# Kernel tuning notes

Hardware: AMD Instinct MI355X
Metric: run time of the kernel (lower is better)

Reference implementation:

```python
import jax, jax.numpy as jnp
import numpy as np

N_NODES = 100000
N_EDGES = 3200000
IN_C, HID_C, OUT_C = 128, 16, 5
NEG_SLOPE = 0.2


def setup_inputs() -> dict:
    key = jax.random.key(0)
    ks = jax.random.split(key, 12)
    x = jax.random.normal(ks[0], (N_NODES, IN_C), dtype=jnp.float32)
    edge_index = jax.random.randint(ks[1], (2, N_EDGES), 0, N_NODES, dtype=jnp.int64)
    # GATConv layer 1 params (heads=1)
    s1 = 1.0 / np.sqrt(IN_C)
    W1 = jax.random.uniform(ks[2], (IN_C, HID_C), jnp.float32, -s1, s1)
    att_src1 = jax.random.uniform(ks[3], (HID_C,), jnp.float32, -1.0, 1.0) * s1
    att_dst1 = jax.random.uniform(ks[4], (HID_C,), jnp.float32, -1.0, 1.0) * s1
    b1 = jnp.zeros((HID_C,), jnp.float32)
    # GATConv layer 2 params
    s2 = 1.0 / np.sqrt(HID_C)
    W2 = jax.random.uniform(ks[5], (HID_C, OUT_C), jnp.float32, -s2, s2)
    att_src2 = jax.random.uniform(ks[6], (OUT_C,), jnp.float32, -1.0, 1.0) * s2
    att_dst2 = jax.random.uniform(ks[7], (OUT_C,), jnp.float32, -1.0, 1.0) * s2
    b2 = jnp.zeros((OUT_C,), jnp.float32)
    return {"x": x, "edge_index": edge_index,
            "W1": W1, "att_src1": att_src1, "att_dst1": att_dst1, "b1": b1,
            "W2": W2, "att_src2": att_src2, "att_dst2": att_dst2, "b2": b2}


def gat_layer(x, src, dst, W, att_src, att_dst, bias, n_nodes):
    # project: [N, C_out]
    h = x @ W
    a_src = h @ att_src  # [N]
    a_dst = h @ att_dst  # [N]
    e = a_src[src] + a_dst[dst]            # [E]
    e = jax.nn.leaky_relu(e, NEG_SLOPE)
    # per-destination-node softmax over incoming edges (stable)
    m = jax.ops.segment_max(e, dst, num_segments=n_nodes)
    ex = jnp.exp(e - m[dst])
    denom = jax.ops.segment_sum(ex, dst, num_segments=n_nodes)
    alpha = ex / (denom[dst] + 1e-16)      # [E]
    # weighted scatter-aggregate of source features
    out = jax.ops.segment_sum(h[src] * alpha[:, None], dst, num_segments=n_nodes)
    return out + bias


def reference(x, edge_index, W1, att_src1, att_dst1, b1, W2, att_src2, att_dst2, b2):
    n = x.shape[0]
    loops = jnp.arange(n, dtype=edge_index.dtype)
    src = jnp.concatenate([edge_index[0], loops])  # add_self_loops=True
    dst = jnp.concatenate([edge_index[1], loops])
    h = gat_layer(x, src, dst, W1, att_src1, att_dst1, b1, n)
    h = jax.nn.relu(h)
    h = gat_layer(h, src, dst, W2, att_src2, att_dst2, b2, n)
    return jax.nn.log_softmax(h, axis=1)
```

## Files before the change

### kernel.cpp

```cpp
#include <hip/hip_runtime.h>
#include <hip/hip_fp16.h>

#define N_NODES 100000
#define N_EDGES 3200000
#define E_TOT   (N_EDGES + N_NODES)
#define IN_C 128
#define HID  16
#define OUTC 5
#define NEG_SLOPE 0.2f

#define NBKT 391
#define CAP  9216
#define P1_TILE 8192
#define P1_GRID ((E_TOT + P1_TILE - 1) / P1_TILE)

__device__ __forceinline__ float pk_half2(float a, float b) {
    __half2 h = __halves2half2(__float2half(a), __float2half(b));
    return *(float*)&h;
}
__device__ __forceinline__ float2 unpk_half2(float v) {
    return __half22float2(*(__half2*)&v);
}

__global__ void zero_gcnt_k(int* __restrict__ gcnt) {
    int i = blockIdx.x * blockDim.x + threadIdx.x;
    if (i < NBKT) gcnt[i] = 0;
}

__global__ __launch_bounds__(256) void part_k(const int* __restrict__ ei,
                                              int* __restrict__ gcnt,
                                              unsigned* __restrict__ pairs) {
    __shared__ unsigned vbuf[P1_TILE];
    __shared__ unsigned short bbuf[P1_TILE];
    __shared__ int hist[NBKT];
    __shared__ int cur[NBKT];
    int t = threadIdx.x;
    for (int i = t; i < NBKT; i += 256) hist[i] = 0;
    __syncthreads();
    int base = blockIdx.x * P1_TILE;
    int lim = E_TOT - base; if (lim > P1_TILE) lim = P1_TILE;
    for (int i = t; i < lim; i += 256) {
        int e = base + i;
        int s, d;
        if (e < N_EDGES) { s = ei[e]; d = ei[N_EDGES + e]; }
        else             { s = e - N_EDGES; d = s; }
        int b = d >> 8;
        vbuf[i] = ((unsigned)s << 8) | (unsigned)(d & 255);
        bbuf[i] = (unsigned short)b;
        atomicAdd(&hist[b], 1);
    }
    __syncthreads();
    for (int i = t; i < NBKT; i += 256) {
        int h = hist[i];
        cur[i] = h ? atomicAdd(&gcnt[i], h) : 0;
    }
    __syncthreads();
    for (int i = t; i < lim; i += 256) {
        int b = bbuf[i];
        int p = atomicAdd(&cur[b], 1);
        if (p >= 0 && p < CAP) pairs[(size_t)b * CAP + p] = vbuf[i];
    }
}

__global__ void scan_gcnt_k(const int* __restrict__ gcnt, int* __restrict__ cbase) {
    __shared__ int s[512];
    int t = threadIdx.x;
    int v = (t < NBKT) ? gcnt[t] : 0;
    s[t] = v; __syncthreads();
    for (int off = 1; off < 512; off <<= 1) {
        int x = (t >= off) ? s[t - off] : 0;
        __syncthreads();
        s[t] += x;
        __syncthreads();
    }
    if (t < NBKT) cbase[t] = s[t] - v;
}

__global__ __launch_bounds__(256) void build_k(const unsigned* __restrict__ pairs,
                                               const int* __restrict__ gcnt,
                                               const int* __restrict__ cbase,
                                               int* __restrict__ csr,
                                               int* __restrict__ row_start,
                                               int* __restrict__ cnt) {
    __shared__ int c[256], s[256], cur[256];
    int t = threadIdx.x;
    int b = blockIdx.x;
    c[t] = 0;
    __syncthreads();
    int tot = gcnt[b];
    if (tot > CAP) tot = CAP;
    size_t pbase = (size_t)b * CAP;
    for (int i = t; i < tot; i += 256) atomicAdd(&c[pairs[pbase + i] & 255u], 1);
    __syncthreads();
    int v0 = c[t];
    s[t] = v0; __syncthreads();
    for (int off = 1; off < 256; off <<= 1) {
        int x = (t >= off) ? s[t - off] : 0;
        __syncthreads();
        s[t] += x;
        __syncthreads();
    }
    int excl = s[t] - v0;
    int gbase = cbase[b];
    int node = (b << 8) + t;
    if (node < N_NODES) { row_start[node] = gbase + excl; cnt[node] = v0; }
    cur[t] = gbase + excl;
    __syncthreads();
    for (int i = t; i < tot; i += 256) {
        unsigned v = pairs[pbase + i];
        int pos = atomicAdd(&cur[v & 255u], 1);
        csr[pos] = (int)(v >> 8);
    }
}

__global__ void proj1_k(const float* __restrict__ x, const float* __restrict__ W1,
                        const float* __restrict__ att_s, const float* __restrict__ att_d,
                        __half* __restrict__ h1f, float* __restrict__ a_src,
                        float* __restrict__ a_dst) {
    __shared__ float sW[IN_C * HID];
    __shared__ float sX[16 * IN_C];
    __shared__ float sH[16 * HID];
    int t = threadIdx.x;
    for (int i = t; i < IN_C * HID; i += 256) sW[i] = W1[i];
    int node0 = blockIdx.x * 16;
    for (int i = t; i < 16 * IN_C; i += 256) {
        int r = i >> 7, c = i & 127;
        int node = node0 + r;
        sX[i] = (node < N_NODES) ? x[(size_t)node * IN_C + c] : 0.0f;
    }
    __syncthreads();
    int r = t >> 4, c = t & 15;
    int node = node0 + r;
    float acc = 0.0f;
    #pragma unroll 8
    for (int k = 0; k < IN_C; ++k) acc += sX[r * IN_C + k] * sW[k * HID + c];
    sH[r * HID + c] = acc;
    if (node < N_NODES) h1f[(size_t)node * HID + c] = __float2half(acc);
    __syncthreads();
    if (c == 0 && node < N_NODES) {
        float s = 0.0f, d = 0.0f;
        #pragma unroll
        for (int k = 0; k < HID; ++k) {
            float hv = sH[r * HID + k];
            s += hv * att_s[k];
            d += hv * att_d[k];
        }
        a_src[node] = s;
        a_dst[node] = d;
    }
}

__global__ __launch_bounds__(256) void gat1_k(
    const int* __restrict__ csr, const int* __restrict__ row_start,
    const int* __restrict__ cnt, const __half* __restrict__ h1f,
    const float* __restrict__ a_src1, const float* __restrict__ a_dst1,
    const float* __restrict__ b1, const float* __restrict__ W2,
    const float* __restrict__ as2, const float* __restrict__ ad2,
    float4* __restrict__ h2p, float* __restrict__ a_dst2) {
    __shared__ float sW2[HID * OUTC];
    __shared__ float sB1[HID];
    __shared__ float sAs[OUTC], sAd[OUTC];
    int t = threadIdx.x;
    if (t < HID * OUTC) sW2[t] = W2[t];
    if (t < HID) sB1[t] = b1[t];
    if (t < OUTC) { sAs[t] = as2[t]; sAd[t] = ad2[t]; }
    __syncthreads();

    int node = (blockIdx.x * 256 + t) >> 4;
    int lane = t & 15;
    int start = row_start[node];
    int len   = cnt[node];
    float ad  = a_dst1[node];

    float acc[HID];
    #pragma unroll
    for (int c = 0; c < HID; ++c) acc[c] = 0.0f;
    float accd = 0.0f;
    for (int it = lane; it < len; it += 16) {
        int s = csr[start + it];
        float v = a_src1[s] + ad;
        v = (v > 0.0f) ? v : NEG_SLOPE * v;
        float ex = __expf(v);
        accd += ex;
        const float4* hp = (const float4*)(h1f + (size_t)s * HID);
        float4 r0 = hp[0], r1 = hp[1];
        float2 f0 = unpk_half2(r0.x), f1 = unpk_half2(r0.y);
        float2 f2 = unpk_half2(r0.z), f3 = unpk_half2(r0.w);
        float2 f4 = unpk_half2(r1.x), f5 = unpk_half2(r1.y);
        float2 f6 = unpk_half2(r1.z), f7 = unpk_half2(r1.w);
        acc[0]  += ex * f0.x; acc[1]  += ex * f0.y;
        acc[2]  += ex * f1.x; acc[3]  += ex * f1.y;
        acc[4]  += ex * f2.x; acc[5]  += ex * f2.y;
        acc[6]  += ex * f3.x; acc[7]  += ex * f3.y;
        acc[8]  += ex * f4.x; acc[9]  += ex * f4.y;
        acc[10] += ex * f5.x; acc[11] += ex * f5.y;
        acc[12] += ex * f6.x; acc[13] += ex * f6.y;
        acc[14] += ex * f7.x; acc[15] += ex * f7.y;
    }
    #pragma unroll
    for (int off = 8; off; off >>= 1) {
        accd += __shfl_xor(accd, off);
        #pragma unroll
        for (int c = 0; c < HID; ++c) acc[c] += __shfl_xor(acc[c], off);
    }
    if (lane == 0) {
        float inv = 1.0f / (accd + 1e-16f);
        float g[HID];
        #pragma unroll
        for (int k = 0; k < HID; ++k) g[k] = fmaxf(acc[k] * inv + sB1[k], 0.0f);
        float h2[OUTC];
        #pragma unroll
        for (int c = 0; c < OUTC; ++c) {
            float a = 0.0f;
            #pragma unroll
            for (int k = 0; k < HID; ++k) a += g[k] * sW2[k * OUTC + c];
            h2[c] = a;
        }
        float s2 = 0.0f, d2 = 0.0f;
        #pragma unroll
        for (int c = 0; c < OUTC; ++c) { s2 += h2[c] * sAs[c]; d2 += h2[c] * sAd[c]; }
        a_dst2[node] = d2;
        float4 r;
        r.x = s2;
        r.y = pk_half2(h2[0], h2[1]);
        r.z = pk_half2(h2[2], h2[3]);
        r.w = pk_half2(h2[4], 0.0f);
        h2p[node] = r;
    }
}

__global__ __launch_bounds__(256) void gat2_k(
    const int* __restrict__ csr, const int* __restrict__ row_start,
    const int* __restrict__ cnt, const float4* __restrict__ h2p,
    const float* __restrict__ a_dst2, const float* __restrict__ b2,
    float* __restrict__ out) {
    __shared__ float sB2[OUTC];
    int t = threadIdx.x;
    if (t < OUTC) sB2[t] = b2[t];
    __syncthreads();

    int node = (blockIdx.x * 256 + t) >> 4;
    int lane = t & 15;
    int start = row_start[node];
    int len   = cnt[node];
    float ad  = a_dst2[node];

    float acc[OUTC];
    #pragma unroll
    for (int c = 0; c < OUTC; ++c) acc[c] = 0.0f;
    float accd = 0.0f;
    for (int it = lane; it < len; it += 16) {
        int s = csr[start + it];
        float4 r = h2p[s];
        float v = r.x + ad;
        v = (v > 0.0f) ? v : NEG_SLOPE * v;
        float ex = __expf(v);
        accd += ex;
        float2 f01 = unpk_half2(r.y);
        float2 f23 = unpk_half2(r.z);
        float2 f4_ = unpk_half2(r.w);
        acc[0] += ex * f01.x; acc[1] += ex * f01.y;
        acc[2] += ex * f23.x; acc[3] += ex * f23.y;
        acc[4] += ex * f4_.x;
    }
    #pragma unroll
    for (int off = 8; off; off >>= 1) {
        accd += __shfl_xor(accd, off);
        #pragma unroll
        for (int c = 0; c < OUTC; ++c) acc[c] += __shfl_xor(acc[c], off);
    }
    if (lane == 0) {
        float inv = 1.0f / (accd + 1e-16f);
        float val[OUTC];
        float mx = -3.4e38f;
        #pragma unroll
        for (int c = 0; c < OUTC; ++c) {
            val[c] = acc[c] * inv + sB2[c];
            mx = fmaxf(mx, val[c]);
        }
        float se = 0.0f;
        #pragma unroll
        for (int c = 0; c < OUTC; ++c) se += __expf(val[c] - mx);
        float lse = logf(se) + mx;
        #pragma unroll
        for (int c = 0; c < OUTC; ++c)
            out[(size_t)node * OUTC + c] = val[c] - lse;
    }
}

extern "C" void kernel_launch(void* const* d_in, const int* in_sizes, int n_in,
                              void* d_out, int out_size, void* d_ws, size_t ws_size,
                              hipStream_t stream) {
    const float* x    = (const float*)d_in[0];
    const int*   ei   = (const int*)d_in[1];
    const float* W1   = (const float*)d_in[2];
    const float* as1  = (const float*)d_in[3];
    const float* ad1  = (const float*)d_in[4];
    const float* b1   = (const float*)d_in[5];
    const float* W2   = (const float*)d_in[6];
    const float* as2  = (const float*)d_in[7];
    const float* ad2  = (const float*)d_in[8];
    const float* b2   = (const float*)d_in[9];
    float* out = (float*)d_out;

    char* wsb = (char*)d_ws;
    unsigned* pairs = (unsigned*)wsb;
    __half* h1f     = (__half*)wsb;
    float4* h2p     = (float4*)(wsb + 3200000);
    float*  asrc1   = (float*)(wsb + 4800000);
    float*  adst1   = asrc1 + N_NODES;
    float*  adst2   = adst1 + N_NODES;
    int* csr       = (int*)(wsb + (size_t)NBKT * CAP * 4);
    int* cnt       = csr + E_TOT;
    int* row_start = cnt + N_NODES;
    int* gcnt      = row_start + N_NODES;
    int* cbase     = gcnt + NBKT;

    const int B = 256;
    const int gW = (N_NODES * 16) / B;

    zero_gcnt_k<<<(NBKT + B - 1) / B, B, 0, stream>>>(gcnt);
    part_k<<<P1_GRID, B, 0, stream>>>(ei, gcnt, pairs);
    scan_gcnt_k<<<1, 512, 0, stream>>>(gcnt, cbase);
    build_k<<<NBKT, B, 0, stream>>>(pairs, gcnt, cbase, csr, row_start, cnt);

    proj1_k<<<(N_NODES + 15) / 16, 256, 0, stream>>>(x, W1, as1, ad1, h1f, asrc1, adst1);
    gat1_k<<<gW, B, 0, stream>>>(csr, row_start, cnt, h1f, asrc1, adst1, b1,
                                 W2, as2, ad2, h2p, adst2);
    gat2_k<<<gW, B, 0, stream>>>(csr, row_start, cnt, h2p, adst2, b2, out);
}
```

Before: 274.3 us.

## Drop global CSR build; bucket-local CSR in shared memory inside GAT kernels

Removes the scan and build kernels and the global CSR arrays. Each GAT layer now rebuilds a per-half-bucket CSR in LDS from the partitioned pairs, then aggregates. The edge partition and the layer-1 projection are merged into one launch as disjoint block ranges, and the projection now loads with float4. This trades the global CSR write and read plus two launches for redundant pair scans in both layers, a HCAP limit in LDS, and only 782 blocks per aggregation kernel, which means lower parallelism and more LDS per block.

```diff
diff --git a/kernel.cpp b/kernel.cpp
--- a/kernel.cpp
+++ b/kernel.cpp
@@ -11,8 +11,10 @@
 
 #define NBKT 391
 #define CAP  9216
-#define P1_TILE 8192
-#define P1_GRID ((E_TOT + P1_TILE - 1) / P1_TILE)
+#define HCAP 4736
+#define P_TILE 8192
+#define PART_GRID ((E_TOT + P_TILE - 1) / P_TILE)
+#define PROJ_GRID ((N_NODES + 15) / 16)
 
 __device__ __forceinline__ float pk_half2(float a, float b) {
     __half2 h = __halves2half2(__float2half(a), __float2half(b));
@@ -27,264 +29,298 @@
     if (i < NBKT) gcnt[i] = 0;
 }
 
-__global__ __launch_bounds__(256) void part_k(const int* __restrict__ ei,
-                                              int* __restrict__ gcnt,
-                                              unsigned* __restrict__ pairs) {
-    __shared__ unsigned vbuf[P1_TILE];
-    __shared__ unsigned short bbuf[P1_TILE];
-    __shared__ int hist[NBKT];
-    __shared__ int cur[NBKT];
+__global__ __launch_bounds__(256) void partproj_k(
+    const int* __restrict__ ei, int* __restrict__ gcnt, unsigned* __restrict__ pairs,
+    const float* __restrict__ x, const float* __restrict__ W1,
+    const float* __restrict__ att_s, const float* __restrict__ att_d,
+    __half* __restrict__ h1f, float* __restrict__ a_src, float* __restrict__ a_dst) {
+    __shared__ __align__(16) char smem[52288];
     int t = threadIdx.x;
-    for (int i = t; i < NBKT; i += 256) hist[i] = 0;
-    __syncthreads();
-    int base = blockIdx.x * P1_TILE;
-    int lim = E_TOT - base; if (lim > P1_TILE) lim = P1_TILE;
-    for (int i = t; i < lim; i += 256) {
-        int e = base + i;
-        int s, d;
-        if (e < N_EDGES) { s = ei[e]; d = ei[N_EDGES + e]; }
-        else             { s = e - N_EDGES; d = s; }
-        int b = d >> 8;
-        vbuf[i] = ((unsigned)s << 8) | (unsigned)(d & 255);
-        bbuf[i] = (unsigned short)b;
-        atomicAdd(&hist[b], 1);
-    }
-    __syncthreads();
-    for (int i = t; i < NBKT; i += 256) {
-        int h = hist[i];
-        cur[i] = h ? atomicAdd(&gcnt[i], h) : 0;
-    }
-    __syncthreads();
-    for (int i = t; i < lim; i += 256) {
-        int b = bbuf[i];
-        int p = atomicAdd(&cur[b], 1);
-        if (p >= 0 && p < CAP) pairs[(size_t)b * CAP + p] = vbuf[i];
-    }
-}
-
-__global__ void scan_gcnt_k(const int* __restrict__ gcnt, int* __restrict__ cbase) {
-    __shared__ int s[512];
-    int t = threadIdx.x;
-    int v = (t < NBKT) ? gcnt[t] : 0;
-    s[t] = v; __syncthreads();
-    for (int off = 1; off < 512; off <<= 1) {
-        int x = (t >= off) ? s[t - off] : 0;
-        __syncthreads();
-        s[t] += x;
-        __syncthreads();
-    }
-    if (t < NBKT) cbase[t] = s[t] - v;
-}
-
-__global__ __launch_bounds__(256) void build_k(const unsigned* __restrict__ pairs,
-                                               const int* __restrict__ gcnt,
-                                               const int* __restrict__ cbase,
-                                               int* __restrict__ csr,
-                                               int* __restrict__ row_start,
-                                               int* __restrict__ cnt) {
-    __shared__ int c[256], s[256], cur[256];
-    int t = threadIdx.x;
-    int b = blockIdx.x;
-    c[t] = 0;
-    __syncthreads();
-    int tot = gcnt[b];
-    if (tot > CAP) tot = CAP;
-    size_t pbase = (size_t)b * CAP;
-    for (int i = t; i < tot; i += 256) atomicAdd(&c[pairs[pbase + i] & 255u], 1);
-    __syncthreads();
-    int v0 = c[t];
-    s[t] = v0; __syncthreads();
-    for (int off = 1; off < 256; off <<= 1) {
-        int x = (t >= off) ? s[t - off] : 0;
-        __syncthreads();
-        s[t] += x;
-        __syncthreads();
-    }
-    int excl = s[t] - v0;
-    int gbase = cbase[b];
-    int node = (b << 8) + t;
-    if (node < N_NODES) { row_start[node] = gbase + excl; cnt[node] = v0; }
-    cur[t] = gbase + excl;
-    __syncthreads();
-    for (int i = t; i < tot; i += 256) {
-        unsigned v = pairs[pbase + i];
-        int pos = atomicAdd(&cur[v & 255u], 1);
-        csr[pos] = (int)(v >> 8);
-    }
-}
-
-__global__ void proj1_k(const float* __restrict__ x, const float* __restrict__ W1,
-                        const float* __restrict__ att_s, const float* __restrict__ att_d,
-                        __half* __restrict__ h1f, float* __restrict__ a_src,
-                        float* __restrict__ a_dst) {
-    __shared__ float sW[IN_C * HID];
-    __shared__ float sX[16 * IN_C];
-    __shared__ float sH[16 * HID];
-    int t = threadIdx.x;
-    for (int i = t; i < IN_C * HID; i += 256) sW[i] = W1[i];
-    int node0 = blockIdx.x * 16;
-    for (int i = t; i < 16 * IN_C; i += 256) {
-        int r = i >> 7, c = i & 127;
+    if (blockIdx.x < PART_GRID) {
+        unsigned* vbuf       = (unsigned*)smem;
+        unsigned short* bbuf = (unsigned short*)(smem + 32768);
+        int* hist            = (int*)(smem + 49152);
+        int* cur             = (int*)(smem + 50716);
+        for (int i = t; i < NBKT; i += 256) hist[i] = 0;
+        __syncthreads();
+        int base = blockIdx.x * P_TILE;
+        int lim = E_TOT - base; if (lim > P_TILE) lim = P_TILE;
+        for (int i = t; i < lim; i += 256) {
+            int e = base + i;
+            int s, d;
+            if (e < N_EDGES) { s = ei[e]; d = ei[N_EDGES + e]; }
+            else             { s = e - N_EDGES; d = s; }
+            int b = d >> 8;
+            vbuf[i] = ((unsigned)s << 8) | (unsigned)(d & 255);
+            bbuf[i] = (unsigned short)b;
+            atomicAdd(&hist[b], 1);
+        }
+        __syncthreads();
+        for (int i = t; i < NBKT; i += 256) {
+            int h = hist[i];
+            cur[i] = h ? atomicAdd(&gcnt[i], h) : 0;
+        }
+        __syncthreads();
+        for (int i = t; i < lim; i += 256) {
+            int b = bbuf[i];
+            int p = atomicAdd(&cur[b], 1);
+            if (p >= 0 && p < CAP) pairs[(size_t)b * CAP + p] = vbuf[i];
+        }
+    } else {
+        float* sW = (float*)smem;
+        float* sX = (float*)(smem + 8192);
+        float* sH = (float*)(smem + 16384);
+        int bid = blockIdx.x - PART_GRID;
+        const float4* W4 = (const float4*)W1;
+        for (int i = t; i < IN_C * HID / 4; i += 256) ((float4*)sW)[i] = W4[i];
+        int node0 = bid * 16;
+        const float4* x4 = (const float4*)x;
+        for (int i = t; i < 16 * IN_C / 4; i += 256) {
+            int r = i >> 5, c4 = i & 31;
+            int node = node0 + r;
+            float4 v = make_float4(0.f, 0.f, 0.f, 0.f);
+            if (node < N_NODES) v = x4[(size_t)node * 32 + c4];
+            *((float4*)&sX[r * IN_C + c4 * 4]) = v;
+        }
+        __syncthreads();
+        int r = t >> 4, c = t & 15;
         int node = node0 + r;
-        sX[i] = (node < N_NODES) ? x[(size_t)node * IN_C + c] : 0.0f;
-    }
-    __syncthreads();
-    int r = t >> 4, c = t & 15;
-    int node = node0 + r;
-    float acc = 0.0f;
-    #pragma unroll 8
-    for (int k = 0; k < IN_C; ++k) acc += sX[r * IN_C + k] * sW[k * HID + c];
-    sH[r * HID + c] = acc;
-    if (node < N_NODES) h1f[(size_t)node * HID + c] = __float2half(acc);
-    __syncthreads();
-    if (c == 0 && node < N_NODES) {
-        float s = 0.0f, d = 0.0f;
-        #pragma unroll
-        for (int k = 0; k < HID; ++k) {
-            float hv = sH[r * HID + k];
-            s += hv * att_s[k];
-            d += hv * att_d[k];
-        }
-        a_src[node] = s;
-        a_dst[node] = d;
-    }
-}
-
-__global__ __launch_bounds__(256) void gat1_k(
-    const int* __restrict__ csr, const int* __restrict__ row_start,
-    const int* __restrict__ cnt, const __half* __restrict__ h1f,
-    const float* __restrict__ a_src1, const float* __restrict__ a_dst1,
-    const float* __restrict__ b1, const float* __restrict__ W2,
-    const float* __restrict__ as2, const float* __restrict__ ad2,
-    float4* __restrict__ h2p, float* __restrict__ a_dst2) {
+        float acc = 0.0f;
+        #pragma unroll 8
+        for (int k = 0; k < IN_C; ++k) acc += sX[r * IN_C + k] * sW[k * HID + c];
+        sH[r * HID + c] = acc;
+        if (node < N_NODES) h1f[(size_t)node * HID + c] = __float2half(acc);
+        __syncthreads();
+        if (c == 0 && node < N_NODES) {
+            float s = 0.0f, d = 0.0f;
+            #pragma unroll
+            for (int k = 0; k < HID; ++k) {
+                float hv = sH[r * HID + k];
+                s += hv * att_s[k];
+                d += hv * att_d[k];
+            }
+            a_src[node] = s;
+            a_dst[node] = d;
+        }
+    }
+}
+
+__global__ __launch_bounds__(256) void gat1s_k(
+    const unsigned* __restrict__ pairs, const int* __restrict__ gcnt,
+    const __half* __restrict__ h1f, const float* __restrict__ asrc1,
+    const float* __restrict__ adst1, const float* __restrict__ b1,
+    const float* __restrict__ W2, const float* __restrict__ as2,
+    const float* __restrict__ ad2, float4* __restrict__ h2p,
+    float* __restrict__ adst2) {
+    __shared__ int ccnt[128], sexc[128], cur[128];
+    __shared__ int lcsr[HCAP];
+    __shared__ float adt[128];
     __shared__ float sW2[HID * OUTC];
     __shared__ float sB1[HID];
     __shared__ float sAs[OUTC], sAd[OUTC];
     int t = threadIdx.x;
+    int parent = blockIdx.x >> 1, half = blockIdx.x & 1;
+    if (t < 128) ccnt[t] = 0;
+    else {
+        int idx = t - 128;
+        int node = (parent << 8) + (half << 7) + idx;
+        adt[idx] = (node < N_NODES) ? adst1[node] : 0.0f;
+    }
     if (t < HID * OUTC) sW2[t] = W2[t];
     if (t < HID) sB1[t] = b1[t];
     if (t < OUTC) { sAs[t] = as2[t]; sAd[t] = ad2[t]; }
     __syncthreads();
-
-    int node = (blockIdx.x * 256 + t) >> 4;
-    int lane = t & 15;
-    int start = row_start[node];
-    int len   = cnt[node];
-    float ad  = a_dst1[node];
-
-    float acc[HID];
-    #pragma unroll
-    for (int c = 0; c < HID; ++c) acc[c] = 0.0f;
-    float accd = 0.0f;
-    for (int it = lane; it < len; it += 16) {
-        int s = csr[start + it];
-        float v = a_src1[s] + ad;
-        v = (v > 0.0f) ? v : NEG_SLOPE * v;
-        float ex = __expf(v);
-        accd += ex;
-        const float4* hp = (const float4*)(h1f + (size_t)s * HID);
-        float4 r0 = hp[0], r1 = hp[1];
-        float2 f0 = unpk_half2(r0.x), f1 = unpk_half2(r0.y);
-        float2 f2 = unpk_half2(r0.z), f3 = unpk_half2(r0.w);
-        float2 f4 = unpk_half2(r1.x), f5 = unpk_half2(r1.y);
-        float2 f6 = unpk_half2(r1.z), f7 = unpk_half2(r1.w);
-        acc[0]  += ex * f0.x; acc[1]  += ex * f0.y;
-        acc[2]  += ex * f1.x; acc[3]  += ex * f1.y;
-        acc[4]  += ex * f2.x; acc[5]  += ex * f2.y;
-        acc[6]  += ex * f3.x; acc[7]  += ex * f3.y;
-        acc[8]  += ex * f4.x; acc[9]  += ex * f4.y;
-        acc[10] += ex * f5.x; acc[11] += ex * f5.y;
-        acc[12] += ex * f6.x; acc[13] += ex * f6.y;
-        acc[14] += ex * f7.x; acc[15] += ex * f7.y;
-    }
-    #pragma unroll
-    for (int off = 8; off; off >>= 1) {
-        accd += __shfl_xor(accd, off);
+    int tot = gcnt[parent]; if (tot > CAP) tot = CAP; if (tot < 0) tot = 0;
+    size_t pb = (size_t)parent * CAP;
+    for (int i = t; i < tot; i += 256) {
+        unsigned v = pairs[pb + i];
+        int dl = (int)(v & 255u);
+        if ((dl >> 7) == half) atomicAdd(&ccnt[dl & 127], 1);
+    }
+    __syncthreads();
+    if (t < 128) sexc[t] = ccnt[t];
+    __syncthreads();
+    for (int off = 1; off < 128; off <<= 1) {
+        int xv = 0;
+        if (t < 128 && t >= off) xv = sexc[t - off];
+        __syncthreads();
+        if (t < 128) sexc[t] += xv;
+        __syncthreads();
+    }
+    if (t < 128) { int e = sexc[t] - ccnt[t]; sexc[t] = e; cur[t] = e; }
+    __syncthreads();
+    for (int i = t; i < tot; i += 256) {
+        unsigned v = pairs[pb + i];
+        int dl = (int)(v & 255u);
+        if ((dl >> 7) == half) {
+            int pos = atomicAdd(&cur[dl & 127], 1);
+            if (pos < HCAP) lcsr[pos] = (int)(v >> 8);
+        }
+    }
+    __syncthreads();
+    int g = t >> 4, lane = t & 15;
+    for (int batch = 0; batch < 8; ++batch) {
+        int nl = batch * 16 + g;
+        int node = (parent << 8) + (half << 7) + nl;
+        int start = sexc[nl];
+        int len = ccnt[nl];
+        if (start > HCAP) start = HCAP;
+        if (start + len > HCAP) len = HCAP - start;
+        float ad = adt[nl];
+        float acc[HID];
         #pragma unroll
-        for (int c = 0; c < HID; ++c) acc[c] += __shfl_xor(acc[c], off);
-    }
-    if (lane == 0) {
-        float inv = 1.0f / (accd + 1e-16f);
-        float g[HID];
+        for (int c = 0; c < HID; ++c) acc[c] = 0.0f;
+        float accd = 0.0f;
+        for (int it = lane; it < len; it += 16) {
+            int s = lcsr[start + it];
+            float v = asrc1[s] + ad;
+            v = (v > 0.0f) ? v : NEG_SLOPE * v;
+            float ex = __expf(v);
+            accd += ex;
+            const float4* hp = (const float4*)(h1f + (size_t)s * HID);
+            float4 r0 = hp[0], r1 = hp[1];
+            float2 f0 = unpk_half2(r0.x), f1 = unpk_half2(r0.y);
+            float2 f2 = unpk_half2(r0.z), f3 = unpk_half2(r0.w);
+            float2 f4 = unpk_half2(r1.x), f5 = unpk_half2(r1.y);
+            float2 f6 = unpk_half2(r1.z), f7 = unpk_half2(r1.w);
+            acc[0]  += ex * f0.x; acc[1]  += ex * f0.y;
+            acc[2]  += ex * f1.x; acc[3]  += ex * f1.y;
+            acc[4]  += ex * f2.x; acc[5]  += ex * f2.y;
+            acc[6]  += ex * f3.x; acc[7]  += ex * f3.y;
+            acc[8]  += ex * f4.x; acc[9]  += ex * f4.y;
+            acc[10] += ex * f5.x; acc[11] += ex * f5.y;
+            acc[12] += ex * f6.x; acc[13] += ex * f6.y;
+            acc[14] += ex * f7.x; acc[15] += ex * f7.y;
+        }
         #pragma unroll
-        for (int k = 0; k < HID; ++k) g[k] = fmaxf(acc[k] * inv + sB1[k], 0.0f);
-        float h2[OUTC];
-        #pragma unroll
-        for (int c = 0; c < OUTC; ++c) {
-            float a = 0.0f;
-            #pragma unroll
-            for (int k = 0; k < HID; ++k) a += g[k] * sW2[k * OUTC + c];
-            h2[c] = a;
-        }
-        float s2 = 0.0f, d2 = 0.0f;
-        #pragma unroll
-        for (int c = 0; c < OUTC; ++c) { s2 += h2[c] * sAs[c]; d2 += h2[c] * sAd[c]; }
-        a_dst2[node] = d2;
-        float4 r;
-        r.x = s2;
-        r.y = pk_half2(h2[0], h2[1]);
-        r.z = pk_half2(h2[2], h2[3]);
-        r.w = pk_half2(h2[4], 0.0f);
-        h2p[node] = r;
-    }
-}
-
-__global__ __launch_bounds__(256) void gat2_k(
-    const int* __restrict__ csr, const int* __restrict__ row_start,
-    const int* __restrict__ cnt, const float4* __restrict__ h2p,
-    const float* __restrict__ a_dst2, const float* __restrict__ b2,
-    float* __restrict__ out) {
+        for (int off = 8; off; off >>= 1) {
+            accd += __shfl_xor(accd, off);
+            #pragma unroll
+            for (int c = 0; c < HID; ++c) acc[c] += __shfl_xor(acc[c], off);
+        }
+        if (lane == 0 && node < N_NODES) {
+            float inv = 1.0f / (accd + 1e-16f);
+            float gg[HID];
+            #pragma unroll
+            for (int k = 0; k < HID; ++k) gg[k] = fmaxf(acc[k] * inv + sB1[k], 0.0f);
+            float h2[OUTC];
+            #pragma unroll
+            for (int c = 0; c < OUTC; ++c) {
+                float a = 0.0f;
+                #pragma unroll
+                for (int k = 0; k < HID; ++k) a += gg[k] * sW2[k * OUTC + c];
+                h2[c] = a;
+            }
+            float s2 = 0.0f, d2 = 0.0f;
+            #pragma unroll
+            for (int c = 0; c < OUTC; ++c) { s2 += h2[c] * sAs[c]; d2 += h2[c] * sAd[c]; }
+            adst2[node] = d2;
+            float4 r;
+            r.x = s2;
+            r.y = pk_half2(h2[0], h2[1]);
+            r.z = pk_half2(h2[2], h2[3]);
+            r.w = pk_half2(h2[4], 0.0f);
+            h2p[node] = r;
+        }
+    }
+}
+
+__global__ __launch_bounds__(256) void gat2s_k(
+    const unsigned* __restrict__ pairs, const int* __restrict__ gcnt,
+    const float4* __restrict__ h2p, const float* __restrict__ adst2,
+    const float* __restrict__ b2, float* __restrict__ out) {
+    __shared__ int ccnt[128], sexc[128], cur[128];
+    __shared__ int lcsr[HCAP];
+    __shared__ float adt[128];
     __shared__ float sB2[OUTC];
     int t = threadIdx.x;
+    int parent = blockIdx.x >> 1, half = blockIdx.x & 1;
+    if (t < 128) ccnt[t] = 0;
+    else {
+        int idx = t - 128;
+        int node = (parent << 8) + (half << 7) + idx;
+        adt[idx] = (node < N_NODES) ? adst2[node] : 0.0f;
+    }
     if (t < OUTC) sB2[t] = b2[t];
     __syncthreads();
-
-    int node = (blockIdx.x * 256 + t) >> 4;
-    int lane = t & 15;
-    int start = row_start[node];
-    int len   = cnt[node];
-    float ad  = a_dst2[node];
-
-    float acc[OUTC];
-    #pragma unroll
-    for (int c = 0; c < OUTC; ++c) acc[c] = 0.0f;
-    float accd = 0.0f;
-    for (int it = lane; it < len; it += 16) {
-        int s = csr[start + it];
-        float4 r = h2p[s];
-        float v = r.x + ad;
-        v = (v > 0.0f) ? v : NEG_SLOPE * v;
-        float ex = __expf(v);
-        accd += ex;
-        float2 f01 = unpk_half2(r.y);
-        float2 f23 = unpk_half2(r.z);
-        float2 f4_ = unpk_half2(r.w);
-        acc[0] += ex * f01.x; acc[1] += ex * f01.y;
-        acc[2] += ex * f23.x; acc[3] += ex * f23.y;
-        acc[4] += ex * f4_.x;
-    }
-    #pragma unroll
-    for (int off = 8; off; off >>= 1) {
-        accd += __shfl_xor(accd, off);
+    int tot = gcnt[parent]; if (tot > CAP) tot = CAP; if (tot < 0) tot = 0;
+    size_t pb = (size_t)parent * CAP;
+    for (int i = t; i < tot; i += 256) {
+        unsigned v = pairs[pb + i];
+        int dl = (int)(v & 255u);
+        if ((dl >> 7) == half) atomicAdd(&ccnt[dl & 127], 1);
+    }
+    __syncthreads();
+    if (t < 128) sexc[t] = ccnt[t];
+    __syncthreads();
+    for (int off = 1; off < 128; off <<= 1) {
+        int xv = 0;
+        if (t < 128 && t >= off) xv = sexc[t - off];
+        __syncthreads();
+        if (t < 128) sexc[t] += xv;
+        __syncthreads();
+    }
+    if (t < 128) { int e = sexc[t] - ccnt[t]; sexc[t] = e; cur[t] = e; }
+    __syncthreads();
+    for (int i = t; i < tot; i += 256) {
+        unsigned v = pairs[pb + i];
+        int dl = (int)(v & 255u);
+        if ((dl >> 7) == half) {
+            int pos = atomicAdd(&cur[dl & 127], 1);
+            if (pos < HCAP) lcsr[pos] = (int)(v >> 8);
+        }
+    }
+    __syncthreads();
+    int g = t >> 4, lane = t & 15;
+    for (int batch = 0; batch < 8; ++batch) {
+        int nl = batch * 16 + g;
+        int node = (parent << 8) + (half << 7) + nl;
+        int start = sexc[nl];
+        int len = ccnt[nl];
+        if (start > HCAP) start = HCAP;
+        if (start + len > HCAP) len = HCAP - start;
+        float ad = adt[nl];
+        float acc[OUTC];
         #pragma unroll
-        for (int c = 0; c < OUTC; ++c) acc[c] += __shfl_xor(acc[c], off);
-    }
-    if (lane == 0) {
-        float inv = 1.0f / (accd + 1e-16f);
-        float val[OUTC];
-        float mx = -3.4e38f;
+        for (int c = 0; c < OUTC; ++c) acc[c] = 0.0f;
+        float accd = 0.0f;
+        for (int it = lane; it < len; it += 16) {
+            int s = lcsr[start + it];
+            float4 r = h2p[s];
+            float v = r.x + ad;
+            v = (v > 0.0f) ? v : NEG_SLOPE * v;
+            float ex = __expf(v);
+            accd += ex;
+            float2 f01 = unpk_half2(r.y);
+            float2 f23 = unpk_half2(r.z);
+            float2 f4_ = unpk_half2(r.w);
+            acc[0] += ex * f01.x; acc[1] += ex * f01.y;
+            acc[2] += ex * f23.x; acc[3] += ex * f23.y;
+            acc[4] += ex * f4_.x;
+        }
         #pragma unroll
-        for (int c = 0; c < OUTC; ++c) {
-            val[c] = acc[c] * inv + sB2[c];
-            mx = fmaxf(mx, val[c]);
-        }
-        float se = 0.0f;
-        #pragma unroll
-        for (int c = 0; c < OUTC; ++c) se += __expf(val[c] - mx);
-        float lse = logf(se) + mx;
-        #pragma unroll
-        for (int c = 0; c < OUTC; ++c)
-            out[(size_t)node * OUTC + c] = val[c] - lse;
+        for (int off = 8; off; off >>= 1) {
+            accd += __shfl_xor(accd, off);
+            #pragma unroll
+            for (int c = 0; c < OUTC; ++c) acc[c] += __shfl_xor(acc[c], off);
+        }
+        if (lane == 0 && node < N_NODES) {
+            float inv = 1.0f / (accd + 1e-16f);
+            float val[OUTC];
+            float mx = -3.4e38f;
+            #pragma unroll
+            for (int c = 0; c < OUTC; ++c) {
+                val[c] = acc[c] * inv + sB2[c];
+                mx = fmaxf(mx, val[c]);
+            }
+            float se = 0.0f;
+            #pragma unroll
+            for (int c = 0; c < OUTC; ++c) se += __expf(val[c] - mx);
+            float lse = logf(se) + mx;
+            #pragma unroll
+            for (int c = 0; c < OUTC; ++c)
+                out[(size_t)node * OUTC + c] = val[c] - lse;
+        }
     }
 }
 
@@ -305,27 +341,17 @@
 
     char* wsb = (char*)d_ws;
     unsigned* pairs = (unsigned*)wsb;
-    __half* h1f     = (__half*)wsb;
-    float4* h2p     = (float4*)(wsb + 3200000);
-    float*  asrc1   = (float*)(wsb + 4800000);
+    float4* h2p     = (float4*)(wsb + (size_t)NBKT * CAP * 4);
+    __half* h1f     = (__half*)((char*)h2p + (size_t)N_NODES * 16);
+    float*  asrc1   = (float*)((char*)h1f + (size_t)N_NODES * HID * 2);
     float*  adst1   = asrc1 + N_NODES;
     float*  adst2   = adst1 + N_NODES;
-    int* csr       = (int*)(wsb + (size_t)NBKT * CAP * 4);
-    int* cnt       = csr + E_TOT;
-    int* row_start = cnt + N_NODES;
-    int* gcnt      = row_start + N_NODES;
-    int* cbase     = gcnt + NBKT;
-
-    const int B = 256;
-    const int gW = (N_NODES * 16) / B;
-
-    zero_gcnt_k<<<(NBKT + B - 1) / B, B, 0, stream>>>(gcnt);
-    part_k<<<P1_GRID, B, 0, stream>>>(ei, gcnt, pairs);
-    scan_gcnt_k<<<1, 512, 0, stream>>>(gcnt, cbase);
-    build_k<<<NBKT, B, 0, stream>>>(pairs, gcnt, cbase, csr, row_start, cnt);
-
-    proj1_k<<<(N_NODES + 15) / 16, 256, 0, stream>>>(x, W1, as1, ad1, h1f, asrc1, adst1);
-    gat1_k<<<gW, B, 0, stream>>>(csr, row_start, cnt, h1f, asrc1, adst1, b1,
-                                 W2, as2, ad2, h2p, adst2);
-    gat2_k<<<gW, B, 0, stream>>>(csr, row_start, cnt, h2p, adst2, b2, out);
-}
+    int*    gcnt    = (int*)(adst2 + N_NODES);
+
+    zero_gcnt_k<<<(NBKT + 255) / 256, 256, 0, stream>>>(gcnt);
+    partproj_k<<<PART_GRID + PROJ_GRID, 256, 0, stream>>>(
+        ei, gcnt, pairs, x, W1, as1, ad1, h1f, asrc1, adst1);
+    gat1s_k<<<NBKT * 2, 256, 0, stream>>>(pairs, gcnt, h1f, asrc1, adst1, b1,
+                                          W2, as2, ad2, h2p, adst2);
+    gat2s_k<<<NBKT * 2, 256, 0, stream>>>(pairs, gcnt, h2p, adst2, b2, out);
+}
```

New measurement: 276.1 us. Within noise of the previous version (+0.6%).
